# Kernel tuning notes

Hardware: AMD Instinct MI355X
Metric: run time of the kernel (lower is better)

## Reference

```python
import jax, jax.numpy as jnp
import numpy as np

DIM_X, DIM_Y, BATCH = 64, 64, 2


def setup_inputs() -> dict:
    key = jax.random.key(0)
    k1, k2, k3 = jax.random.split(key, 3)
    mean_in = jax.random.normal(k1, (BATCH, DIM_X, DIM_Y), dtype=jnp.float32)
    # std must be positive
    std_in = jax.random.uniform(k2, (BATCH, DIM_X, DIM_Y), dtype=jnp.float32, minval=0.1, maxval=1.0)
    # identity correlation matrix -> PSD covariance, valid sqrt/div downstream
    n = DIM_X * DIM_Y
    corr_in = jnp.broadcast_to(jnp.eye(n, dtype=jnp.float32), (BATCH, n, n))
    # kaiming_uniform_(a=sqrt(5)) on a (dx, dy) weight -> bound = 1/sqrt(dy)
    bound = 1.0 / np.sqrt(DIM_Y)
    weight = jax.random.uniform(k3, (DIM_X, DIM_Y), dtype=jnp.float32, minval=-bound, maxval=bound)
    return {"mean_in": mean_in, "std_in": std_in, "corr_in": corr_in, "weight": weight}


def reference(mean_in, std_in, corr_in, weight):
    B, dx, dy = mean_in.shape
    n = dx * dy
    # fft(fft(w, dim=0), dim=1) == 2D FFT
    wfft = jnp.fft.fft2(weight)  # (dx, dy) complex

    # covariance from std and corr: cov[b,i,j,k,l] = std[b,i,j] * corr[b,i,j,k,l] * std[b,k,l]
    corr = corr_in.reshape(B, dx, dy, dx, dy)
    cov = std_in[:, None, None, :, :] * corr * std_in[:, :, :, None, None]

    # mean path: circular 2D convolution via FFT
    mean_fft = jnp.fft.fft2(mean_in, axes=(1, 2))
    mean_out = jnp.real(jnp.fft.ifft2(wfft[None] * mean_fft, axes=(1, 2)))

    # covariance path: 4D FFT, broadcast multiply by wfft on both index pairs, 4D IFFT
    cov_f = jnp.fft.fftn(cov, axes=(1, 2, 3, 4))
    cov_f = wfft[None, None, None, :, :] * cov_f * wfft[None, :, :, None, None]
    cov_out = jnp.real(jnp.fft.ifftn(cov_f, axes=(1, 2, 3, 4)))
    cov_out = cov_out.reshape(B, n, n)

    # update_correlation: std = sqrt(diag(cov)); corr = cov / (std outer std)
    var = jnp.diagonal(cov_out, axis1=-2, axis2=-1)  # (B, n)
    std_out = jnp.sqrt(jnp.maximum(var, 1e-12))
    denom = std_out[:, :, None] * std_out[:, None, :]
    corr_out = cov_out / denom
    std_out = std_out.reshape(B, dx, dy)
    return mean_out, std_out, corr_out
```

## Files before the change

kernel.cpp:

```cpp
#include <hip/hip_runtime.h>
#include <math.h>

#define DXY   64
#define NN    4096
#define NB    2
#define CP    65

#define C16 0.9238795325112867f
#define S16 0.3826834323650898f
#define R22 0.7071067811865476f

__device__ __forceinline__ void cmul_ip(float2& a, float wr, float wi) {
    float t = a.x * wr - a.y * wi;
    a.y = a.x * wi + a.y * wr;
    a.x = t;
}

__device__ __forceinline__ void bf4(float2* y, int i0, int i1, int i2, int i3, int inv) {
    float2 a0 = y[i0], a1 = y[i1], a2 = y[i2], a3 = y[i3];
    float t0r = a0.x + a2.x, t0i = a0.y + a2.y;
    float t1r = a0.x - a2.x, t1i = a0.y - a2.y;
    float t2r = a1.x + a3.x, t2i = a1.y + a3.y;
    float dr  = a1.x - a3.x, di  = a1.y - a3.y;
    float t3r, t3i;
    if (inv) { t3r = -di; t3i = dr; } else { t3r = di; t3i = -dr; }
    y[i0] = make_float2(t0r + t2r, t0i + t2i);
    y[i1] = make_float2(t1r + t3r, t1i + t3i);
    y[i2] = make_float2(t0r - t2r, t0i - t2i);
    y[i3] = make_float2(t1r - t3r, t1i - t3i);
}

__device__ __forceinline__ void fft16_fwd(float2* y) {
    bf4(y, 0, 4, 8, 12, 0);
    bf4(y, 1, 5, 9, 13, 0);
    cmul_ip(y[5],  C16, -S16); cmul_ip(y[9],  R22, -R22); cmul_ip(y[13],  S16, -C16);
    bf4(y, 2, 6, 10, 14, 0);
    cmul_ip(y[6],  R22, -R22); cmul_ip(y[10], 0.f, -1.f); cmul_ip(y[14], -R22, -R22);
    bf4(y, 3, 7, 11, 15, 0);
    cmul_ip(y[7],  S16, -C16); cmul_ip(y[11], -R22, -R22); cmul_ip(y[15], -C16,  S16);
    bf4(y, 0, 1, 2, 3, 0); bf4(y, 4, 5, 6, 7, 0);
    bf4(y, 8, 9, 10, 11, 0); bf4(y, 12, 13, 14, 15, 0);
}

__device__ __forceinline__ void fft16_inv(float2* y) {
    bf4(y, 0, 1, 2, 3, 1); bf4(y, 4, 5, 6, 7, 1);
    bf4(y, 8, 9, 10, 11, 1); bf4(y, 12, 13, 14, 15, 1);
    cmul_ip(y[5],  C16,  S16); cmul_ip(y[9],  R22,  R22); cmul_ip(y[13],  S16,  C16);
    cmul_ip(y[6],  R22,  R22); cmul_ip(y[10], 0.f,  1.f); cmul_ip(y[14], -R22,  R22);
    cmul_ip(y[7],  S16,  C16); cmul_ip(y[11], -R22,  R22); cmul_ip(y[15], -C16, -S16);
    bf4(y, 0, 4, 8, 12, 1); bf4(y, 1, 5, 9, 13, 1);
    bf4(y, 2, 6, 10, 14, 1); bf4(y, 3, 7, 11, 15, 1);
}

template<int US, int NS, bool FUSEW>
__device__ void fwd_pass(float2* z, const float2* __restrict__ wf, int u, int k1,
                         float c1r, float c1i, float s2, float2 Wb)
{
    const int B = u * US;
    float2 y[16];
    float twr = 1.f, twi = 0.f;
#pragma unroll
    for (int n2 = 0; n2 < 16; ++n2) {
        float2 x0 = z[B + n2 * NS];
        float2 x1 = z[B + (n2 + 16) * NS];
        float2 x2 = z[B + (n2 + 32) * NS];
        float2 x3 = z[B + (n2 + 48) * NS];
        float er  = fmaf(s2, x2.x, x0.x), ei = fmaf(s2, x2.y, x0.y);
        float orr = fmaf(s2, x3.x, x1.x), oi = fmaf(s2, x3.y, x1.y);
        float br = er + c1r * orr - c1i * oi;
        float bi = ei + c1r * oi + c1i * orr;
        y[n2].x = twr * br - twi * bi;
        y[n2].y = twr * bi + twi * br;
        float t = twr * Wb.x - twi * Wb.y;
        twi = twr * Wb.y + twi * Wb.x;
        twr = t;
    }
    fft16_fwd(y);
    if (FUSEW) {
#pragma unroll
        for (int p = 0; p < 16; ++p) {
            float2 wv = wf[(16 * k1 + p) * 64 + u];
            cmul_ip(y[p], wv.x, wv.y);
        }
    }
    __syncthreads();
#pragma unroll
    for (int p = 0; p < 16; ++p) z[B + (16 * k1 + p) * NS] = y[p];
    __syncthreads();
}

template<int US, int NS>
__device__ void inv_pass(float2* z, int u, int k1,
                         float ci1r, float ci1i, float s2, float2 Wbc)
{
    const int B = u * US;
    float2 y[16];
#pragma unroll
    for (int p = 0; p < 16; ++p) y[p] = z[B + (16 * k1 + p) * NS];
    fft16_inv(y);
    float twr = 1.f, twi = 0.f;
#pragma unroll
    for (int n2 = 0; n2 < 16; ++n2) {
        cmul_ip(y[n2], twr, twi);
        float t = twr * Wbc.x - twi * Wbc.y;
        twi = twr * Wbc.y + twi * Wbc.x;
        twr = t;
    }
#pragma unroll
    for (int n2 = 0; n2 < 16; ++n2) z[B + (16 * k1 + n2) * NS] = y[n2];
    __syncthreads();
    float2 xx[16];
#pragma unroll
    for (int n2 = 0; n2 < 16; ++n2) {
        float2 h0 = z[B + n2 * NS];
        float2 h1 = z[B + (n2 + 16) * NS];
        float2 h2 = z[B + (n2 + 32) * NS];
        float2 h3 = z[B + (n2 + 48) * NS];
        float er  = fmaf(s2, h2.x, h0.x), ei = fmaf(s2, h2.y, h0.y);
        float orr = fmaf(s2, h3.x, h1.x), oi = fmaf(s2, h3.y, h1.y);
        xx[n2].x = er + ci1r * orr - ci1i * oi;
        xx[n2].y = ei + ci1r * oi + ci1i * orr;
    }
    __syncthreads();
#pragma unroll
    for (int n2 = 0; n2 < 16; ++n2) z[B + (16 * k1 + n2) * NS] = xx[n2];
    __syncthreads();
}

__global__ __launch_bounds__(256, 4)
void row_conv2_kernel(const float* __restrict__ in, float* __restrict__ out,
                      const float2* __restrict__ wfft_br,
                      const float* __restrict__ sstd, float* var_out)
{
    __shared__ float2 z[64 * CP];
    const int tid = threadIdx.x;
    const int u   = ((tid >> 6) << 4) | (tid & 15);
    const int k1  = (tid >> 4) & 3;
    const float c1r = (k1 == 0) ? 1.f : ((k1 == 2) ? -1.f : 0.f);
    const float c1i = (k1 == 1) ? -1.f : ((k1 == 3) ? 1.f : 0.f);
    const float s2  = (k1 & 1) ? -1.f : 1.f;
    const float ang = -0.09817477042468103f * (float)k1;
    const float2 Wb  = make_float2(cosf(ang), sinf(ang));
    const float2 Wbc = make_float2(Wb.x, -Wb.y);
    const float ci1r = c1r, ci1i = -c1i;

    const int row0 = 2 * blockIdx.x;
    const long long off0 = (long long)row0 * NN, off1 = off0 + NN;
    const int b   = row0 >> 12;
    const int rI0 = row0 & (NN - 1), rI1 = rI0 + 1;
    const float* sb = nullptr;
    float sI0 = 1.f, sI1 = 1.f;
    if (sstd) { sb = sstd + (long long)b * NN; sI0 = sb[rI0]; sI1 = sb[rI1]; }

#pragma unroll
    for (int i = 0; i < 4; ++i) {
        int idx = tid + 256 * i;
        int p = idx * 4;
        int r = p >> 6, c = p & 63;
        float4 a  = *(const float4*)(in + off0 + p);
        float4 cc = *(const float4*)(in + off1 + p);
        if (sb) {
            float4 s4 = *(const float4*)(sb + p);
            a.x *= sI0 * s4.x; a.y *= sI0 * s4.y; a.z *= sI0 * s4.z; a.w *= sI0 * s4.w;
            cc.x *= sI1 * s4.x; cc.y *= sI1 * s4.y; cc.z *= sI1 * s4.z; cc.w *= sI1 * s4.w;
        }
        float2* zp = z + r * CP + c;
        zp[0] = make_float2(a.x, cc.x);
        zp[1] = make_float2(a.y, cc.y);
        zp[2] = make_float2(a.z, cc.z);
        zp[3] = make_float2(a.w, cc.w);
    }
    __syncthreads();

    fwd_pass<CP, 1, false>(z, nullptr,  u, k1, c1r, c1i, s2, Wb);
    fwd_pass<1, CP, true >(z, wfft_br,  u, k1, c1r, c1i, s2, Wb);
    inv_pass<1, CP>(z, u, k1, ci1r, ci1i, s2, Wbc);
    inv_pass<CP, 1>(z, u, k1, ci1r, ci1i, s2, Wbc);

    const float scale = 1.0f / 4096.0f;
#pragma unroll
    for (int i = 0; i < 4; ++i) {
        int idx = tid + 256 * i;
        int p = idx * 4;
        int r = p >> 6, c = p & 63;
        const float2* zp = z + r * CP + c;
        float4 a, cc;
        a.x = zp[0].x * scale; a.y = zp[1].x * scale;
        a.z = zp[2].x * scale; a.w = zp[3].x * scale;
        cc.x = zp[0].y * scale; cc.y = zp[1].y * scale;
        cc.z = zp[2].y * scale; cc.w = zp[3].y * scale;
        *(float4*)(out + off0 + p) = a;
        *(float4*)(out + off1 + p) = cc;
    }
    if (var_out && tid == 0) {
        var_out[row0]     = z[(rI0 >> 6) * CP + (rI0 & 63)].x * scale;
        var_out[row0 + 1] = z[(rI1 >> 6) * CP + (rI1 & 63)].y * scale;
    }
}

__global__ __launch_bounds__(256, 4)
void wfft_kernel(const float* __restrict__ w, float2* wfft_br)
{
    __shared__ float2 z[64 * CP];
    const int tid = threadIdx.x;
    const int u   = ((tid >> 6) << 4) | (tid & 15);
    const int k1  = (tid >> 4) & 3;
    const float c1r = (k1 == 0) ? 1.f : ((k1 == 2) ? -1.f : 0.f);
    const float c1i = (k1 == 1) ? -1.f : ((k1 == 3) ? 1.f : 0.f);
    const float s2  = (k1 & 1) ? -1.f : 1.f;
    const float ang = -0.09817477042468103f * (float)k1;
    const float2 Wb = make_float2(cosf(ang), sinf(ang));

#pragma unroll
    for (int i = 0; i < 16; ++i) {
        int p = tid + 256 * i;
        z[(p >> 6) * CP + (p & 63)] = make_float2(w[p], 0.f);
    }
    __syncthreads();
    fwd_pass<CP, 1, false>(z, nullptr, u, k1, c1r, c1i, s2, Wb);
    fwd_pass<1, CP, false>(z, nullptr, u, k1, c1r, c1i, s2, Wb);
#pragma unroll
    for (int i = 0; i < 16; ++i) {
        int p = tid + 256 * i;
        wfft_br[p] = z[(p >> 6) * CP + (p & 63)];
    }
}

__global__ __launch_bounds__(256)
void transpose_inplace_kernel(float* data)
{
    int bx = blockIdx.x, by = blockIdx.y, b = blockIdx.z;
    if (by > bx) return;
    __shared__ float tA[64 * 65];
    __shared__ float tB[64 * 65];
    const int f  = threadIdx.x & 15;
    const int r0 = threadIdx.x >> 4;
    long long base = (long long)b * NN * NN;
    float* A  = data + base + (long long)(by * 64) * NN + bx * 64;
    float* Bt = data + base + (long long)(bx * 64) * NN + by * 64;
    if (bx == by) {
#pragma unroll
        for (int it = 0; it < 4; ++it) {
            int r = r0 + 16 * it;
            float4 v = *(const float4*)(A + (long long)r * NN + 4 * f);
            tA[(4 * f + 0) * 65 + r] = v.x; tA[(4 * f + 1) * 65 + r] = v.y;
            tA[(4 * f + 2) * 65 + r] = v.z; tA[(4 * f + 3) * 65 + r] = v.w;
        }
        __syncthreads();
#pragma unroll
        for (int it = 0; it < 4; ++it) {
            int c = r0 + 16 * it;
            float4 v;
            v.x = tA[c * 65 + 4 * f + 0]; v.y = tA[c * 65 + 4 * f + 1];
            v.z = tA[c * 65 + 4 * f + 2]; v.w = tA[c * 65 + 4 * f + 3];
            *(float4*)(A + (long long)c * NN + 4 * f) = v;
        }
    } else {
#pragma unroll
        for (int it = 0; it < 4; ++it) {
            int r = r0 + 16 * it;
            float4 v = *(const float4*)(A + (long long)r * NN + 4 * f);
            float4 w = *(const float4*)(Bt + (long long)r * NN + 4 * f);
            tA[(4 * f + 0) * 65 + r] = v.x; tA[(4 * f + 1) * 65 + r] = v.y;
            tA[(4 * f + 2) * 65 + r] = v.z; tA[(4 * f + 3) * 65 + r] = v.w;
            tB[(4 * f + 0) * 65 + r] = w.x; tB[(4 * f + 1) * 65 + r] = w.y;
            tB[(4 * f + 2) * 65 + r] = w.z; tB[(4 * f + 3) * 65 + r] = w.w;
        }
        __syncthreads();
#pragma unroll
        for (int it = 0; it < 4; ++it) {
            int c = r0 + 16 * it;
            float4 v, w;
            v.x = tB[c * 65 + 4 * f + 0]; v.y = tB[c * 65 + 4 * f + 1];
            v.z = tB[c * 65 + 4 * f + 2]; v.w = tB[c * 65 + 4 * f + 3];
            w.x = tA[c * 65 + 4 * f + 0]; w.y = tA[c * 65 + 4 * f + 1];
            w.z = tA[c * 65 + 4 * f + 2]; w.w = tA[c * 65 + 4 * f + 3];
            *(float4*)(A + (long long)c * NN + 4 * f)  = v;
            *(float4*)(Bt + (long long)c * NN + 4 * f) = w;
        }
    }
}

__global__ __launch_bounds__(256)
void norm_transpose_inplace_kernel(float* data, const float* __restrict__ rstd)
{
    int bx = blockIdx.x, by = blockIdx.y, b = blockIdx.z;
    if (by > bx) return;
    __shared__ float tA[64 * 65];
    __shared__ float tB[64 * 65];
    const int f  = threadIdx.x & 15;
    const int r0 = threadIdx.x >> 4;
    long long base = (long long)b * NN * NN;
    const float* rs = rstd + (long long)b * NN;
    float* A  = data + base + (long long)(by * 64) * NN + bx * 64;
    float* Bt = data + base + (long long)(bx * 64) * NN + by * 64;
    float4 rsx_bx = *(const float4*)(rs + bx * 64 + 4 * f);
    float4 rsx_by = *(const float4*)(rs + by * 64 + 4 * f);
    if (bx == by) {
#pragma unroll
        for (int it = 0; it < 4; ++it) {
            int r = r0 + 16 * it;
            float4 v = *(const float4*)(A + (long long)r * NN + 4 * f);
            tA[(4 * f + 0) * 65 + r] = v.x; tA[(4 * f + 1) * 65 + r] = v.y;
            tA[(4 * f + 2) * 65 + r] = v.z; tA[(4 * f + 3) * 65 + r] = v.w;
        }
        __syncthreads();
#pragma unroll
        for (int it = 0; it < 4; ++it) {
            int c = r0 + 16 * it;
            float rr = rs[by * 64 + c];
            float4 v;
            v.x = tA[c * 65 + 4 * f + 0] * rr * rsx_bx.x;
            v.y = tA[c * 65 + 4 * f + 1] * rr * rsx_bx.y;
            v.z = tA[c * 65 + 4 * f + 2] * rr * rsx_bx.z;
            v.w = tA[c * 65 + 4 * f + 3] * rr * rsx_bx.w;
            *(float4*)(A + (long long)c * NN + 4 * f) = v;
        }
    } else {
#pragma unroll
        for (int it = 0; it < 4; ++it) {
            int r = r0 + 16 * it;
            float4 v = *(const float4*)(A + (long long)r * NN + 4 * f);
            float4 w = *(const float4*)(Bt + (long long)r * NN + 4 * f);
            tA[(4 * f + 0) * 65 + r] = v.x; tA[(4 * f + 1) * 65 + r] = v.y;
            tA[(4 * f + 2) * 65 + r] = v.z; tA[(4 * f + 3) * 65 + r] = v.w;
            tB[(4 * f + 0) * 65 + r] = w.x; tB[(4 * f + 1) * 65 + r] = w.y;
            tB[(4 * f + 2) * 65 + r] = w.z; tB[(4 * f + 3) * 65 + r] = w.w;
        }
        __syncthreads();
#pragma unroll
        for (int it = 0; it < 4; ++it) {
            int c = r0 + 16 * it;
            float rA = rs[by * 64 + c];
            float rB = rs[bx * 64 + c];
            float4 v, w;
            v.x = tB[c * 65 + 4 * f + 0] * rA * rsx_bx.x;
            v.y = tB[c * 65 + 4 * f + 1] * rA * rsx_bx.y;
            v.z = tB[c * 65 + 4 * f + 2] * rA * rsx_bx.z;
            v.w = tB[c * 65 + 4 * f + 3] * rA * rsx_bx.w;
            w.x = tA[c * 65 + 4 * f + 0] * rB * rsx_by.x;
            w.y = tA[c * 65 + 4 * f + 1] * rB * rsx_by.y;
            w.z = tA[c * 65 + 4 * f + 2] * rB * rsx_by.z;
            w.w = tA[c * 65 + 4 * f + 3] * rB * rsx_by.w;
            *(float4*)(A + (long long)c * NN + 4 * f)  = v;
            *(float4*)(Bt + (long long)c * NN + 4 * f) = w;
        }
    }
}

__global__ __launch_bounds__(256)
void std_kernel(const float* __restrict__ var, float* std_out, float* rstd, int n)
{
    int i = blockIdx.x * 256 + threadIdx.x;
    if (i < n) {
        float s = sqrtf(fmaxf(var[i], 1e-12f));
        std_out[i] = s;
        rstd[i] = 1.0f / s;
    }
}

extern "C" void kernel_launch(void* const* d_in, const int* in_sizes, int n_in,
                              void* d_out, int out_size, void* d_ws, size_t ws_size,
                              hipStream_t stream)
{
    const float* mean_in = (const float*)d_in[0];
    const float* std_in  = (const float*)d_in[1];
    const float* corr_in = (const float*)d_in[2];
    const float* weight  = (const float*)d_in[3];

    float* out      = (float*)d_out;
    float* mean_out = out;
    float* std_out  = out + 8192;
    float* corr_out = out + 16384;

    float*  ws      = (float*)d_ws;
    float2* wfft_br = (float2*)ws;
    float*  var_ws  = ws + 8192;
    float*  rstd_ws = ws + 16384;

    wfft_kernel<<<1, 256, 0, stream>>>(weight, wfft_br);

    row_conv2_kernel<<<1, 256, 0, stream>>>(mean_in, mean_out, wfft_br,
                                            nullptr, nullptr);

    row_conv2_kernel<<<NB * NN / 2, 256, 0, stream>>>(corr_in, corr_out, wfft_br,
                                                      std_in, nullptr);

    dim3 tg(64, 64, NB);
    transpose_inplace_kernel<<<tg, 256, 0, stream>>>(corr_out);

    row_conv2_kernel<<<NB * NN / 2, 256, 0, stream>>>(corr_out, corr_out, wfft_br,
                                                      nullptr, var_ws);

    std_kernel<<<(NB * NN + 255) / 256, 256, 0, stream>>>(var_ws, std_out,
                                                          rstd_ws, NB * NN);

    norm_transpose_inplace_kernel<<<tg, 256, 0, stream>>>(corr_out, rstd_ws);
}
```

Baseline: 483.5 us.

## Replace in-place transposes with pair-interleaved layout between row and column FFT passes

The first FFT convolution pass now writes its output in a pair-interleaved column layout, so the second pass can read two columns contiguously instead of needing a full in-place transpose kernel. The final normalization becomes a simple elementwise scaling, because cov is symmetric and no transpose back is required. Block IDs are swizzled across the grid to spread memory accesses. This removes two full read-write sweeps over the 128 MB covariance buffer, at the cost of strided 16-byte writes in the first pass.

```diff
diff --git a/kernel.cpp b/kernel.cpp
--- a/kernel.cpp
+++ b/kernel.cpp
@@ -127,10 +127,11 @@
     __syncthreads();
 }
 
+template<int INP, int OUTP>
 __global__ __launch_bounds__(256, 4)
-void row_conv2_kernel(const float* __restrict__ in, float* __restrict__ out,
-                      const float2* __restrict__ wfft_br,
-                      const float* __restrict__ sstd, float* var_out)
+void conv2_kernel(const float* __restrict__ in, float* __restrict__ out,
+                  const float2* __restrict__ wfft_br,
+                  const float* __restrict__ sstd, float* var_out)
 {
     __shared__ float2 z[64 * CP];
     const int tid = threadIdx.x;
@@ -144,31 +145,48 @@
     const float2 Wbc = make_float2(Wb.x, -Wb.y);
     const float ci1r = c1r, ci1i = -c1i;
 
-    const int row0 = 2 * blockIdx.x;
-    const long long off0 = (long long)row0 * NN, off1 = off0 + NN;
-    const int b   = row0 >> 12;
-    const int rI0 = row0 & (NN - 1), rI1 = rI0 + 1;
-    const float* sb = nullptr;
-    float sI0 = 1.f, sI1 = 1.f;
-    if (sstd) { sb = sstd + (long long)b * NN; sI0 = sb[rI0]; sI1 = sb[rI1]; }
-
-#pragma unroll
-    for (int i = 0; i < 4; ++i) {
-        int idx = tid + 256 * i;
-        int p = idx * 4;
-        int r = p >> 6, c = p & 63;
-        float4 a  = *(const float4*)(in + off0 + p);
-        float4 cc = *(const float4*)(in + off1 + p);
-        if (sb) {
-            float4 s4 = *(const float4*)(sb + p);
-            a.x *= sI0 * s4.x; a.y *= sI0 * s4.y; a.z *= sI0 * s4.z; a.w *= sI0 * s4.w;
-            cc.x *= sI1 * s4.x; cc.y *= sI1 * s4.y; cc.z *= sI1 * s4.z; cc.w *= sI1 * s4.w;
-        }
-        float2* zp = z + r * CP + c;
-        zp[0] = make_float2(a.x, cc.x);
-        zp[1] = make_float2(a.y, cc.y);
-        zp[2] = make_float2(a.z, cc.z);
-        zp[3] = make_float2(a.w, cc.w);
+    const int bid = blockIdx.x;
+    const int rid = (gridDim.x >= 8)
+                  ? ((bid & 7) * (gridDim.x >> 3) + (bid >> 3)) : bid;
+    const int row0 = 2 * rid;
+    const int b    = row0 >> 12;
+    const int lr0  = row0 & (NN - 1), lr1 = lr0 + 1;
+    const long long mbase = (long long)b * NN * NN;
+
+    if constexpr (INP == 0) {
+        const long long off0 = (long long)row0 * NN, off1 = off0 + NN;
+        const float* sb = nullptr;
+        float sI0 = 1.f, sI1 = 1.f;
+        if (sstd) { sb = sstd + (long long)b * NN; sI0 = sb[lr0]; sI1 = sb[lr1]; }
+#pragma unroll
+        for (int i = 0; i < 4; ++i) {
+            int idx = tid + 256 * i;
+            int p = idx * 4;
+            int r = p >> 6, c = p & 63;
+            float4 a  = *(const float4*)(in + off0 + p);
+            float4 cc = *(const float4*)(in + off1 + p);
+            if (sb) {
+                float4 s4 = *(const float4*)(sb + p);
+                a.x *= sI0 * s4.x; a.y *= sI0 * s4.y; a.z *= sI0 * s4.z; a.w *= sI0 * s4.w;
+                cc.x *= sI1 * s4.x; cc.y *= sI1 * s4.y; cc.z *= sI1 * s4.z; cc.w *= sI1 * s4.w;
+            }
+            float2* zp = z + r * CP + c;
+            zp[0] = make_float2(a.x, cc.x);
+            zp[1] = make_float2(a.y, cc.y);
+            zp[2] = make_float2(a.z, cc.z);
+            zp[3] = make_float2(a.w, cc.w);
+        }
+    } else {
+        const float* slab = in + mbase + (long long)(lr0 >> 1) * (2 * NN);
+#pragma unroll
+        for (int i = 0; i < 8; ++i) {
+            int t = tid + 256 * i;
+            float4 v = *(const float4*)(slab + t * 4);
+            int I = 2 * t;
+            float2* zp = z + (I >> 6) * CP + (I & 63);
+            zp[0] = make_float2(v.x, v.y);
+            zp[1] = make_float2(v.z, v.w);
+        }
     }
     __syncthreads();
 
@@ -178,23 +196,38 @@
     inv_pass<CP, 1>(z, u, k1, ci1r, ci1i, s2, Wbc);
 
     const float scale = 1.0f / 4096.0f;
-#pragma unroll
-    for (int i = 0; i < 4; ++i) {
-        int idx = tid + 256 * i;
-        int p = idx * 4;
-        int r = p >> 6, c = p & 63;
-        const float2* zp = z + r * CP + c;
-        float4 a, cc;
-        a.x = zp[0].x * scale; a.y = zp[1].x * scale;
-        a.z = zp[2].x * scale; a.w = zp[3].x * scale;
-        cc.x = zp[0].y * scale; cc.y = zp[1].y * scale;
-        cc.z = zp[2].y * scale; cc.w = zp[3].y * scale;
-        *(float4*)(out + off0 + p) = a;
-        *(float4*)(out + off1 + p) = cc;
-    }
-    if (var_out && tid == 0) {
-        var_out[row0]     = z[(rI0 >> 6) * CP + (rI0 & 63)].x * scale;
-        var_out[row0 + 1] = z[(rI1 >> 6) * CP + (rI1 & 63)].y * scale;
+    if constexpr (OUTP == 0) {
+        const long long off0 = (long long)row0 * NN, off1 = off0 + NN;
+#pragma unroll
+        for (int i = 0; i < 4; ++i) {
+            int idx = tid + 256 * i;
+            int p = idx * 4;
+            int r = p >> 6, c = p & 63;
+            const float2* zp = z + r * CP + c;
+            float4 a, cc;
+            a.x = zp[0].x * scale; a.y = zp[1].x * scale;
+            a.z = zp[2].x * scale; a.w = zp[3].x * scale;
+            cc.x = zp[0].y * scale; cc.y = zp[1].y * scale;
+            cc.z = zp[2].y * scale; cc.w = zp[3].y * scale;
+            *(float4*)(out + off0 + p) = a;
+            *(float4*)(out + off1 + p) = cc;
+        }
+        if (var_out && tid == 0) {
+            var_out[row0]     = z[(lr0 >> 6) * CP + (lr0 & 63)].x * scale;
+            var_out[row0 + 1] = z[(lr1 >> 6) * CP + (lr1 & 63)].y * scale;
+        }
+    } else {
+        float* obase = out + mbase + (long long)lr0 * 2;
+#pragma unroll
+        for (int i = 0; i < 8; ++i) {
+            int kp = tid + 256 * i;
+            int K = 2 * kp;
+            const float2* zp = z + (K >> 6) * CP + (K & 63);
+            float2 e0 = zp[0], e1 = zp[1];
+            float4 v = make_float4(e0.x * scale, e1.x * scale,
+                                   e0.y * scale, e1.y * scale);
+            *(float4*)(obase + (long long)kp * (2 * NN)) = v;
+        }
     }
 }
 
@@ -227,128 +260,6 @@
 }
 
 __global__ __launch_bounds__(256)
-void transpose_inplace_kernel(float* data)
-{
-    int bx = blockIdx.x, by = blockIdx.y, b = blockIdx.z;
-    if (by > bx) return;
-    __shared__ float tA[64 * 65];
-    __shared__ float tB[64 * 65];
-    const int f  = threadIdx.x & 15;
-    const int r0 = threadIdx.x >> 4;
-    long long base = (long long)b * NN * NN;
-    float* A  = data + base + (long long)(by * 64) * NN + bx * 64;
-    float* Bt = data + base + (long long)(bx * 64) * NN + by * 64;
-    if (bx == by) {
-#pragma unroll
-        for (int it = 0; it < 4; ++it) {
-            int r = r0 + 16 * it;
-            float4 v = *(const float4*)(A + (long long)r * NN + 4 * f);
-            tA[(4 * f + 0) * 65 + r] = v.x; tA[(4 * f + 1) * 65 + r] = v.y;
-            tA[(4 * f + 2) * 65 + r] = v.z; tA[(4 * f + 3) * 65 + r] = v.w;
-        }
-        __syncthreads();
-#pragma unroll
-        for (int it = 0; it < 4; ++it) {
-            int c = r0 + 16 * it;
-            float4 v;
-            v.x = tA[c * 65 + 4 * f + 0]; v.y = tA[c * 65 + 4 * f + 1];
-            v.z = tA[c * 65 + 4 * f + 2]; v.w = tA[c * 65 + 4 * f + 3];
-            *(float4*)(A + (long long)c * NN + 4 * f) = v;
-        }
-    } else {
-#pragma unroll
-        for (int it = 0; it < 4; ++it) {
-            int r = r0 + 16 * it;
-            float4 v = *(const float4*)(A + (long long)r * NN + 4 * f);
-            float4 w = *(const float4*)(Bt + (long long)r * NN + 4 * f);
-            tA[(4 * f + 0) * 65 + r] = v.x; tA[(4 * f + 1) * 65 + r] = v.y;
-            tA[(4 * f + 2) * 65 + r] = v.z; tA[(4 * f + 3) * 65 + r] = v.w;
-            tB[(4 * f + 0) * 65 + r] = w.x; tB[(4 * f + 1) * 65 + r] = w.y;
-            tB[(4 * f + 2) * 65 + r] = w.z; tB[(4 * f + 3) * 65 + r] = w.w;
-        }
-        __syncthreads();
-#pragma unroll
-        for (int it = 0; it < 4; ++it) {
-            int c = r0 + 16 * it;
-            float4 v, w;
-            v.x = tB[c * 65 + 4 * f + 0]; v.y = tB[c * 65 + 4 * f + 1];
-            v.z = tB[c * 65 + 4 * f + 2]; v.w = tB[c * 65 + 4 * f + 3];
-            w.x = tA[c * 65 + 4 * f + 0]; w.y = tA[c * 65 + 4 * f + 1];
-            w.z = tA[c * 65 + 4 * f + 2]; w.w = tA[c * 65 + 4 * f + 3];
-            *(float4*)(A + (long long)c * NN + 4 * f)  = v;
-            *(float4*)(Bt + (long long)c * NN + 4 * f) = w;
-        }
-    }
-}
-
-__global__ __launch_bounds__(256)
-void norm_transpose_inplace_kernel(float* data, const float* __restrict__ rstd)
-{
-    int bx = blockIdx.x, by = blockIdx.y, b = blockIdx.z;
-    if (by > bx) return;
-    __shared__ float tA[64 * 65];
-    __shared__ float tB[64 * 65];
-    const int f  = threadIdx.x & 15;
-    const int r0 = threadIdx.x >> 4;
-    long long base = (long long)b * NN * NN;
-    const float* rs = rstd + (long long)b * NN;
-    float* A  = data + base + (long long)(by * 64) * NN + bx * 64;
-    float* Bt = data + base + (long long)(bx * 64) * NN + by * 64;
-    float4 rsx_bx = *(const float4*)(rs + bx * 64 + 4 * f);
-    float4 rsx_by = *(const float4*)(rs + by * 64 + 4 * f);
-    if (bx == by) {
-#pragma unroll
-        for (int it = 0; it < 4; ++it) {
-            int r = r0 + 16 * it;
-            float4 v = *(const float4*)(A + (long long)r * NN + 4 * f);
-            tA[(4 * f + 0) * 65 + r] = v.x; tA[(4 * f + 1) * 65 + r] = v.y;
-            tA[(4 * f + 2) * 65 + r] = v.z; tA[(4 * f + 3) * 65 + r] = v.w;
-        }
-        __syncthreads();
-#pragma unroll
-        for (int it = 0; it < 4; ++it) {
-            int c = r0 + 16 * it;
-            float rr = rs[by * 64 + c];
-            float4 v;
-            v.x = tA[c * 65 + 4 * f + 0] * rr * rsx_bx.x;
-            v.y = tA[c * 65 + 4 * f + 1] * rr * rsx_bx.y;
-            v.z = tA[c * 65 + 4 * f + 2] * rr * rsx_bx.z;
-            v.w = tA[c * 65 + 4 * f + 3] * rr * rsx_bx.w;
-            *(float4*)(A + (long long)c * NN + 4 * f) = v;
-        }
-    } else {
-#pragma unroll
-        for (int it = 0; it < 4; ++it) {
-            int r = r0 + 16 * it;
-            float4 v = *(const float4*)(A + (long long)r * NN + 4 * f);
-            float4 w = *(const float4*)(Bt + (long long)r * NN + 4 * f);
-            tA[(4 * f + 0) * 65 + r] = v.x; tA[(4 * f + 1) * 65 + r] = v.y;
-            tA[(4 * f + 2) * 65 + r] = v.z; tA[(4 * f + 3) * 65 + r] = v.w;
-            tB[(4 * f + 0) * 65 + r] = w.x; tB[(4 * f + 1) * 65 + r] = w.y;
-            tB[(4 * f + 2) * 65 + r] = w.z; tB[(4 * f + 3) * 65 + r] = w.w;
-        }
-        __syncthreads();
-#pragma unroll
-        for (int it = 0; it < 4; ++it) {
-            int c = r0 + 16 * it;
-            float rA = rs[by * 64 + c];
-            float rB = rs[bx * 64 + c];
-            float4 v, w;
-            v.x = tB[c * 65 + 4 * f + 0] * rA * rsx_bx.x;
-            v.y = tB[c * 65 + 4 * f + 1] * rA * rsx_bx.y;
-            v.z = tB[c * 65 + 4 * f + 2] * rA * rsx_bx.z;
-            v.w = tB[c * 65 + 4 * f + 3] * rA * rsx_bx.w;
-            w.x = tA[c * 65 + 4 * f + 0] * rB * rsx_by.x;
-            w.y = tA[c * 65 + 4 * f + 1] * rB * rsx_by.y;
-            w.z = tA[c * 65 + 4 * f + 2] * rB * rsx_by.z;
-            w.w = tA[c * 65 + 4 * f + 3] * rB * rsx_by.w;
-            *(float4*)(A + (long long)c * NN + 4 * f)  = v;
-            *(float4*)(Bt + (long long)c * NN + 4 * f) = w;
-        }
-    }
-}
-
-__global__ __launch_bounds__(256)
 void std_kernel(const float* __restrict__ var, float* std_out, float* rstd, int n)
 {
     int i = blockIdx.x * 256 + threadIdx.x;
@@ -359,6 +270,21 @@
     }
 }
 
+__global__ __launch_bounds__(256)
+void normalize_kernel(float* data, const float* __restrict__ rstd)
+{
+    long long idx = ((long long)blockIdx.x * 256 + threadIdx.x) * 4;
+    int bb = (int)(idx >> 24);
+    int e  = (int)(idx & (long long)(NN * NN - 1));
+    int a  = e >> 12, c = e & (NN - 1);
+    const float* rs = rstd + bb * NN;
+    float  ra = rs[a];
+    float4 rb = *(const float4*)(rs + c);
+    float4 v  = *(float4*)(data + idx);
+    v.x *= ra * rb.x; v.y *= ra * rb.y; v.z *= ra * rb.z; v.w *= ra * rb.w;
+    *(float4*)(data + idx) = v;
+}
+
 extern "C" void kernel_launch(void* const* d_in, const int* in_sizes, int n_in,
                               void* d_out, int out_size, void* d_ws, size_t ws_size,
                               hipStream_t stream)
@@ -380,20 +306,17 @@
 
     wfft_kernel<<<1, 256, 0, stream>>>(weight, wfft_br);
 
-    row_conv2_kernel<<<1, 256, 0, stream>>>(mean_in, mean_out, wfft_br,
-                                            nullptr, nullptr);
-
-    row_conv2_kernel<<<NB * NN / 2, 256, 0, stream>>>(corr_in, corr_out, wfft_br,
-                                                      std_in, nullptr);
-
-    dim3 tg(64, 64, NB);
-    transpose_inplace_kernel<<<tg, 256, 0, stream>>>(corr_out);
-
-    row_conv2_kernel<<<NB * NN / 2, 256, 0, stream>>>(corr_out, corr_out, wfft_br,
-                                                      nullptr, var_ws);
+    conv2_kernel<0, 0><<<1, 256, 0, stream>>>(mean_in, mean_out, wfft_br,
+                                              nullptr, nullptr);
+
+    conv2_kernel<0, 1><<<NB * NN / 2, 256, 0, stream>>>(corr_in, corr_out,
+                                                        wfft_br, std_in, nullptr);
+
+    conv2_kernel<1, 0><<<NB * NN / 2, 256, 0, stream>>>(corr_out, corr_out,
+                                                        wfft_br, nullptr, var_ws);
 
     std_kernel<<<(NB * NN + 255) / 256, 256, 0, stream>>>(var_ws, std_out,
                                                           rstd_ws, NB * NN);
 
-    norm_transpose_inplace_kernel<<<tg, 256, 0, stream>>>(corr_out, rstd_ws);
-}
+    normalize_kernel<<<NB * NN * (NN / 1024), 256, 0, stream>>>(corr_out, rstd_ws);
+}
```

Result: slower. 520.0 us (+7.5%).

## Replace final normalize-transpose with a plain row normalize by exploiting symmetry

Applied to the files above, without the earlier changes.

The output covariance is symmetric, so the final in-place transpose is dropped. A simple row-wise normalize kernel scales each element by rstd[row]*rstd[col], which removes the tiled shared-memory transpose and its strided accesses. Separately, global loads in the row FFT kernel and the remaining transpose are batched into registers before the shared-memory stores, for more memory-level parallelism, and the transpose gets a launch-bounds occupancy hint. The symmetry assumption can introduce small floating-point differences from the exact transposed result.

```diff
diff --git a/kernel.cpp b/kernel.cpp
--- a/kernel.cpp
+++ b/kernel.cpp
@@ -152,17 +152,29 @@
     float sI0 = 1.f, sI1 = 1.f;
     if (sstd) { sb = sstd + (long long)b * NN; sI0 = sb[rI0]; sI1 = sb[rI1]; }
 
-#pragma unroll
-    for (int i = 0; i < 4; ++i) {
-        int idx = tid + 256 * i;
-        int p = idx * 4;
+    float4 a4[4], c4[4], s4[4];
+#pragma unroll
+    for (int i = 0; i < 4; ++i) {
+        int p = (tid + 256 * i) * 4;
+        a4[i] = *(const float4*)(in + off0 + p);
+        c4[i] = *(const float4*)(in + off1 + p);
+    }
+    if (sb) {
+#pragma unroll
+        for (int i = 0; i < 4; ++i) {
+            int p = (tid + 256 * i) * 4;
+            s4[i] = *(const float4*)(sb + p);
+        }
+    }
+#pragma unroll
+    for (int i = 0; i < 4; ++i) {
+        int p = (tid + 256 * i) * 4;
         int r = p >> 6, c = p & 63;
-        float4 a  = *(const float4*)(in + off0 + p);
-        float4 cc = *(const float4*)(in + off1 + p);
+        float4 a = a4[i], cc = c4[i];
         if (sb) {
-            float4 s4 = *(const float4*)(sb + p);
-            a.x *= sI0 * s4.x; a.y *= sI0 * s4.y; a.z *= sI0 * s4.z; a.w *= sI0 * s4.w;
-            cc.x *= sI1 * s4.x; cc.y *= sI1 * s4.y; cc.z *= sI1 * s4.z; cc.w *= sI1 * s4.w;
+            float4 s = s4[i];
+            a.x *= sI0 * s.x; a.y *= sI0 * s.y; a.z *= sI0 * s.z; a.w *= sI0 * s.w;
+            cc.x *= sI1 * s.x; cc.y *= sI1 * s.y; cc.z *= sI1 * s.z; cc.w *= sI1 * s.w;
         }
         float2* zp = z + r * CP + c;
         zp[0] = make_float2(a.x, cc.x);
@@ -226,7 +238,7 @@
     }
 }
 
-__global__ __launch_bounds__(256)
+__global__ __launch_bounds__(256, 4)
 void transpose_inplace_kernel(float* data)
 {
     int bx = blockIdx.x, by = blockIdx.y, b = blockIdx.z;
@@ -239,12 +251,17 @@
     float* A  = data + base + (long long)(by * 64) * NN + bx * 64;
     float* Bt = data + base + (long long)(bx * 64) * NN + by * 64;
     if (bx == by) {
+        float4 va[4];
 #pragma unroll
         for (int it = 0; it < 4; ++it) {
             int r = r0 + 16 * it;
-            float4 v = *(const float4*)(A + (long long)r * NN + 4 * f);
-            tA[(4 * f + 0) * 65 + r] = v.x; tA[(4 * f + 1) * 65 + r] = v.y;
-            tA[(4 * f + 2) * 65 + r] = v.z; tA[(4 * f + 3) * 65 + r] = v.w;
+            va[it] = *(const float4*)(A + (long long)r * NN + 4 * f);
+        }
+#pragma unroll
+        for (int it = 0; it < 4; ++it) {
+            int r = r0 + 16 * it;
+            tA[(4 * f + 0) * 65 + r] = va[it].x; tA[(4 * f + 1) * 65 + r] = va[it].y;
+            tA[(4 * f + 2) * 65 + r] = va[it].z; tA[(4 * f + 3) * 65 + r] = va[it].w;
         }
         __syncthreads();
 #pragma unroll
@@ -256,94 +273,36 @@
             *(float4*)(A + (long long)c * NN + 4 * f) = v;
         }
     } else {
+        float4 va[4], wb[4];
 #pragma unroll
         for (int it = 0; it < 4; ++it) {
             int r = r0 + 16 * it;
-            float4 v = *(const float4*)(A + (long long)r * NN + 4 * f);
-            float4 w = *(const float4*)(Bt + (long long)r * NN + 4 * f);
-            tA[(4 * f + 0) * 65 + r] = v.x; tA[(4 * f + 1) * 65 + r] = v.y;
-            tA[(4 * f + 2) * 65 + r] = v.z; tA[(4 * f + 3) * 65 + r] = v.w;
-            tB[(4 * f + 0) * 65 + r] = w.x; tB[(4 * f + 1) * 65 + r] = w.y;
-            tB[(4 * f + 2) * 65 + r] = w.z; tB[(4 * f + 3) * 65 + r] = w.w;
+            va[it] = *(const float4*)(A  + (long long)r * NN + 4 * f);
+            wb[it] = *(const float4*)(Bt + (long long)r * NN + 4 * f);
+        }
+#pragma unroll
+        for (int it = 0; it < 4; ++it) {
+            int r = r0 + 16 * it;
+            tA[(4 * f + 0) * 65 + r] = va[it].x; tA[(4 * f + 1) * 65 + r] = va[it].y;
+            tA[(4 * f + 2) * 65 + r] = va[it].z; tA[(4 * f + 3) * 65 + r] = va[it].w;
+            tB[(4 * f + 0) * 65 + r] = wb[it].x; tB[(4 * f + 1) * 65 + r] = wb[it].y;
+            tB[(4 * f + 2) * 65 + r] = wb[it].z; tB[(4 * f + 3) * 65 + r] = wb[it].w;
         }
         __syncthreads();
+        float4 ov[4], ow[4];
 #pragma unroll
         for (int it = 0; it < 4; ++it) {
             int c = r0 + 16 * it;
-            float4 v, w;
-            v.x = tB[c * 65 + 4 * f + 0]; v.y = tB[c * 65 + 4 * f + 1];
-            v.z = tB[c * 65 + 4 * f + 2]; v.w = tB[c * 65 + 4 * f + 3];
-            w.x = tA[c * 65 + 4 * f + 0]; w.y = tA[c * 65 + 4 * f + 1];
-            w.z = tA[c * 65 + 4 * f + 2]; w.w = tA[c * 65 + 4 * f + 3];
-            *(float4*)(A + (long long)c * NN + 4 * f)  = v;
-            *(float4*)(Bt + (long long)c * NN + 4 * f) = w;
-        }
-    }
-}
-
-__global__ __launch_bounds__(256)
-void norm_transpose_inplace_kernel(float* data, const float* __restrict__ rstd)
-{
-    int bx = blockIdx.x, by = blockIdx.y, b = blockIdx.z;
-    if (by > bx) return;
-    __shared__ float tA[64 * 65];
-    __shared__ float tB[64 * 65];
-    const int f  = threadIdx.x & 15;
-    const int r0 = threadIdx.x >> 4;
-    long long base = (long long)b * NN * NN;
-    const float* rs = rstd + (long long)b * NN;
-    float* A  = data + base + (long long)(by * 64) * NN + bx * 64;
-    float* Bt = data + base + (long long)(bx * 64) * NN + by * 64;
-    float4 rsx_bx = *(const float4*)(rs + bx * 64 + 4 * f);
-    float4 rsx_by = *(const float4*)(rs + by * 64 + 4 * f);
-    if (bx == by) {
-#pragma unroll
-        for (int it = 0; it < 4; ++it) {
-            int r = r0 + 16 * it;
-            float4 v = *(const float4*)(A + (long long)r * NN + 4 * f);
-            tA[(4 * f + 0) * 65 + r] = v.x; tA[(4 * f + 1) * 65 + r] = v.y;
-            tA[(4 * f + 2) * 65 + r] = v.z; tA[(4 * f + 3) * 65 + r] = v.w;
-        }
-        __syncthreads();
+            ov[it].x = tB[c * 65 + 4 * f + 0]; ov[it].y = tB[c * 65 + 4 * f + 1];
+            ov[it].z = tB[c * 65 + 4 * f + 2]; ov[it].w = tB[c * 65 + 4 * f + 3];
+            ow[it].x = tA[c * 65 + 4 * f + 0]; ow[it].y = tA[c * 65 + 4 * f + 1];
+            ow[it].z = tA[c * 65 + 4 * f + 2]; ow[it].w = tA[c * 65 + 4 * f + 3];
+        }
 #pragma unroll
         for (int it = 0; it < 4; ++it) {
             int c = r0 + 16 * it;
-            float rr = rs[by * 64 + c];
-            float4 v;
-            v.x = tA[c * 65 + 4 * f + 0] * rr * rsx_bx.x;
-            v.y = tA[c * 65 + 4 * f + 1] * rr * rsx_bx.y;
-            v.z = tA[c * 65 + 4 * f + 2] * rr * rsx_bx.z;
-            v.w = tA[c * 65 + 4 * f + 3] * rr * rsx_bx.w;
-            *(float4*)(A + (long long)c * NN + 4 * f) = v;
-        }
-    } else {
-#pragma unroll
-        for (int it = 0; it < 4; ++it) {
-            int r = r0 + 16 * it;
-            float4 v = *(const float4*)(A + (long long)r * NN + 4 * f);
-            float4 w = *(const float4*)(Bt + (long long)r * NN + 4 * f);
-            tA[(4 * f + 0) * 65 + r] = v.x; tA[(4 * f + 1) * 65 + r] = v.y;
-            tA[(4 * f + 2) * 65 + r] = v.z; tA[(4 * f + 3) * 65 + r] = v.w;
-            tB[(4 * f + 0) * 65 + r] = w.x; tB[(4 * f + 1) * 65 + r] = w.y;
-            tB[(4 * f + 2) * 65 + r] = w.z; tB[(4 * f + 3) * 65 + r] = w.w;
-        }
-        __syncthreads();
-#pragma unroll
-        for (int it = 0; it < 4; ++it) {
-            int c = r0 + 16 * it;
-            float rA = rs[by * 64 + c];
-            float rB = rs[bx * 64 + c];
-            float4 v, w;
-            v.x = tB[c * 65 + 4 * f + 0] * rA * rsx_bx.x;
-            v.y = tB[c * 65 + 4 * f + 1] * rA * rsx_bx.y;
-            v.z = tB[c * 65 + 4 * f + 2] * rA * rsx_bx.z;
-            v.w = tB[c * 65 + 4 * f + 3] * rA * rsx_bx.w;
-            w.x = tA[c * 65 + 4 * f + 0] * rB * rsx_by.x;
-            w.y = tA[c * 65 + 4 * f + 1] * rB * rsx_by.y;
-            w.z = tA[c * 65 + 4 * f + 2] * rB * rsx_by.z;
-            w.w = tA[c * 65 + 4 * f + 3] * rB * rsx_by.w;
-            *(float4*)(A + (long long)c * NN + 4 * f)  = v;
-            *(float4*)(Bt + (long long)c * NN + 4 * f) = w;
+            *(float4*)(A  + (long long)c * NN + 4 * f) = ov[it];
+            *(float4*)(Bt + (long long)c * NN + 4 * f) = ow[it];
         }
     }
 }
@@ -359,6 +318,32 @@
     }
 }
 
+__global__ __launch_bounds__(256)
+void normalize_kernel(float* data, const float* __restrict__ rstd)
+{
+    const int tid = threadIdx.x;
+    const int al  = blockIdx.x;
+    const int bb  = al >> 12, a = al & (NN - 1);
+    const float* rs = rstd + (long long)bb * NN;
+    const float ra = rs[a];
+    float* row = data + (long long)al * NN;
+    float4 v[4], rb[4];
+#pragma unroll
+    for (int i = 0; i < 4; ++i) {
+        int c = tid * 4 + 1024 * i;
+        v[i]  = *(float4*)(row + c);
+        rb[i] = *(const float4*)(rs + c);
+    }
+#pragma unroll
+    for (int i = 0; i < 4; ++i) {
+        int c = tid * 4 + 1024 * i;
+        float4 t = v[i];
+        t.x *= ra * rb[i].x; t.y *= ra * rb[i].y;
+        t.z *= ra * rb[i].z; t.w *= ra * rb[i].w;
+        *(float4*)(row + c) = t;
+    }
+}
+
 extern "C" void kernel_launch(void* const* d_in, const int* in_sizes, int n_in,
                               void* d_out, int out_size, void* d_ws, size_t ws_size,
                               hipStream_t stream)
@@ -395,5 +380,5 @@
     std_kernel<<<(NB * NN + 255) / 256, 256, 0, stream>>>(var_ws, std_out,
                                                           rstd_ws, NB * NN);
 
-    norm_transpose_inplace_kernel<<<tg, 256, 0, stream>>>(corr_out, rstd_ws);
-}
+    normalize_kernel<<<NB * NN, 256, 0, stream>>>(corr_out, rstd_ws);
+}
```

New measurement: 462.6 us. 4.3% less time.
